# Optimization experiments

Measured on AMD Instinct MI355X. Metric: run time of the kernel, lower is better.

## Reference

```python
import jax, jax.numpy as jnp
import numpy as np

TAU = 2.0
V_TH = 1.0
V_RST = 0.0
BN_EPS = 1e-5

# --- ATan surrogate-gradient Heaviside spike (spikingjelly default, alpha=2) ---
@jax.custom_vjp
def atan_spike(x):
    return (x >= 0.0).astype(x.dtype)

def _atan_fwd(x):
    return atan_spike(x), x

def _atan_bwd(x, g):
    alpha = 2.0
    return (g * (alpha / 2.0) / (1.0 + (jnp.pi / 2.0 * alpha * x) ** 2),)

atan_spike.defvjp(_atan_fwd, _atan_bwd)

# --- multi-step LIF (decay_input=False, hard reset, detach_reset=True) ---
def lif(x_seq):
    def step(v, xt):
        v = v - (v - V_RST) / TAU + xt            # charge
        s = atan_spike(v - V_TH)                  # fire
        sd = jax.lax.stop_gradient(s)             # detach_reset
        v = (1.0 - sd) * v + sd * V_RST           # hard reset
        return v, s
    v0 = jnp.full(x_seq.shape[1:], V_RST, x_seq.dtype)
    _, spikes = jax.lax.scan(step, v0, x_seq)
    return spikes

def setup_inputs() -> dict:
    key = jax.random.key(0)
    k1, k2 = jax.random.split(key)
    T, B, N = 64, 256, 512
    x = jax.random.normal(k1, (T, B, N), dtype=jnp.float32)
    # xavier-uniform-like init for Linear weight [out, in]
    bound = float(np.sqrt(6.0 / (N + N)))
    W = jax.random.uniform(k2, (N, N), minval=-bound, maxval=bound, dtype=jnp.float32)
    gamma = jnp.ones((N,), jnp.float32)
    beta = jnp.zeros((N,), jnp.float32)
    return {"x": x, "W": W, "gamma": gamma, "beta": beta}

def reference(x, W, gamma, beta):
    # x: [T, B, N]
    T, B, N = x.shape
    # spatial / temporal spiking gates (reduction='mean')
    spatial = lif(x.mean(axis=-1, keepdims=True))   # [T, B, 1]
    temporal = lif(x.mean(axis=0, keepdims=True))   # [1, B, N] (scan over length-1 T)
    s = (x * spatial) * (x * temporal)
    x = x + s
    x = lif(x)
    # Linear (no bias): y = x @ W.T
    x = jnp.einsum('tbn,mn->tbm', x, W)
    # BatchNorm1d over channels N, stats over flattened T*B (training mode)
    xf = x.reshape(T * B, N)
    mu = xf.mean(axis=0)
    var = xf.var(axis=0)
    xf = (xf - mu) * jax.lax.rsqrt(var + BN_EPS) * gamma + beta
    x = xf.reshape(T, B, N)
    x = lif(x)
    return x
```

## Files before the change

### kernel.cpp

```cpp
#include <hip/hip_runtime.h>
#include <hip/hip_bf16.h>
#include <math.h>

#define TT 64
#define BB 256
#define NN 512

typedef __attribute__((ext_vector_type(8)))  short s16x8;
typedef __attribute__((ext_vector_type(16))) float f32x16;

__device__ __forceinline__ void gload16(const void* g, void* l) {
  __builtin_amdgcn_global_load_lds(
      (const __attribute__((address_space(1))) unsigned int*)g,
      (__attribute__((address_space(3))) unsigned int*)l, 16, 0, 0);
}


__global__ __launch_bounds__(256) void wprep_kernel(
    const float* __restrict__ W, unsigned short* __restrict__ WT) {
  int i = blockIdx.x * 256 + threadIdx.x;
  int m = i >> 9, k = i & 511;
  float v = W[i];
  unsigned u0 = __float_as_uint(v);
  unsigned h0 = (u0 + 0x7FFFu + ((u0 >> 16) & 1u)) >> 16;
  float f0 = __uint_as_float(h0 << 16);
  float r1 = v - f0;
  unsigned u1 = __float_as_uint(r1);
  unsigned h1 = (u1 + 0x7FFFu + ((u1 >> 16) & 1u)) >> 16;
  float f1 = __uint_as_float(h1 << 16);
  float r2 = r1 - f1;
  unsigned u2 = __float_as_uint(r2);
  unsigned h2 = (u2 + 0x7FFFu + ((u2 >> 16) & 1u)) >> 16;
  int cg = m >> 5, kc = k >> 4;
  size_t base = ((size_t)cg * 32 + kc) * 512
              + ((m & 31) + 32 * ((k >> 3) & 1)) * 8 + (k & 7);
  WT[base         ] = (unsigned short)h0;
  WT[base + 262144] = (unsigned short)h1;
  WT[base + 524288] = (unsigned short)h2;
}

__global__ __launch_bounds__(512) void frontend_kernel(
    const float* __restrict__ x, unsigned short* __restrict__ spkT) {
  extern __shared__ float xs[];
  __shared__ float rms[TT];
  __shared__ float sp[TT];
  int b = blockIdx.x, tid = threadIdx.x;
  int l = tid & 63, w = tid >> 6;
  #pragma unroll
  for (int p = 0; p < 16; ++p) {
    int f = p * 512 + tid;
    int t = f >> 7, c4 = f & 127;
    gload16(x + (size_t)t * (BB * NN) + (size_t)b * NN + c4 * 4,
            (char*)xs + p * 8192 + w * 1024);
  }
  __syncthreads();
  #pragma unroll
  for (int j = 0; j < 8; ++j) {
    int t = w * 8 + j;
    float s = 0.f;
    #pragma unroll
    for (int q = 0; q < 8; ++q) s += xs[t * 512 + q * 64 + l];
    #pragma unroll
    for (int off = 32; off; off >>= 1) s += __shfl_xor(s, off);
    if (l == 0) rms[t] = s;
  }
  float cs = 0.f;
  for (int t = 0; t < TT; ++t) cs += xs[t * 512 + tid];
  __syncthreads();
  if (w == 0) {
    float myrm = rms[l];
    float v = 0.f;
    unsigned long long mask = 0ull;
    #pragma unroll
    for (int t = 0; t < TT; ++t) {
      float m = __shfl(myrm, t) * (1.0f / 512.0f);
      v = v * 0.5f + m;
      if (v >= 1.0f) { mask |= (1ull << t); v = 0.f; }
    }
    sp[l] = (float)((mask >> l) & 1ull);
  }
  __syncthreads();
  float te = (cs * (1.0f / 64.0f) >= 1.0f) ? 1.0f : 0.0f;
  float v = 0.f;
  unsigned short* sb = spkT + (size_t)(b >> 5) * 16384 + (tid >> 4) * 512
                     + (b & 31) * 8 + ((tid >> 3) & 1) * 256 + (tid & 7);
  for (int t = 0; t < TT; ++t) {
    float xv = xs[t * 512 + tid];
    float a = xv + (xv * sp[t]) * (xv * te);
    v = v * 0.5f + a;
    unsigned short s = (v >= 1.0f) ? 0x3F80 : 0;
    sb[(size_t)t * 131072] = s;
    if (s) v = 0.f;
  }
}

__global__ __launch_bounds__(256) void gemm_kernel(
    const unsigned short* __restrict__ AT, const unsigned short* __restrict__ WT,
    float* __restrict__ C, float* __restrict__ pS, float* __restrict__ pQ) {
  __shared__ unsigned char sm[2][32768];
  int tid = threadIdx.x;
  int l = tid & 63, w = tid >> 6;
  int wr = w >> 1, wc = w & 1;
  int bx = blockIdx.x, by = blockIdx.y;
  int row0 = bx * 128, col0 = by * 128;
  int lr = l & 31, lh = l >> 5;

  f32x16 acc[2][2];
  #pragma unroll
  for (int f = 0; f < 2; ++f)
    #pragma unroll
    for (int g = 0; g < 2; ++g)
      #pragma unroll
      for (int j = 0; j < 16; ++j) acc[f][g][j] = 0.f;

  auto STAGE = [&](unsigned char* lbase, int kt) {
    #pragma unroll
    for (int j = 0; j < 2; ++j) {
      int c = j * 4 + w;
      int rg = bx * 4 + (c >> 1), kc = kt * 2 + (c & 1);
      gload16((const char*)AT + ((size_t)rg * 32 + kc) * 1024 + l * 16,
              lbase + c * 1024);
    }
    #pragma unroll
    for (int j = 0; j < 6; ++j) {
      int c = j * 4 + w;
      int comp = c >> 3, cg = (c >> 1) & 3, kc = kt * 2 + (c & 1);
      gload16((const char*)WT + (((size_t)comp * 16 + by * 4 + cg) * 32 + kc) * 1024 + l * 16,
              lbase + 8192 + c * 1024);
    }
  };

  STAGE(sm[0], 0);
  #pragma unroll
  for (int kt = 0; kt < 16; ++kt) {
    asm volatile("s_waitcnt lgkmcnt(0)" ::: "memory");
    asm volatile("s_waitcnt vmcnt(0)" ::: "memory");
    asm volatile("s_barrier" ::: "memory");
    if (kt < 15) STAGE(sm[(kt + 1) & 1], kt + 1);
    const unsigned char* bp = sm[kt & 1];
    #pragma unroll
    for (int kc2 = 0; kc2 < 2; ++kc2) {
      s16x8 a[2], bf[2][3];
      #pragma unroll
      for (int f = 0; f < 2; ++f)
        a[f] = *(const s16x8*)(bp + ((wr * 2 + f) * 2 + kc2) * 1024 + l * 16);
      #pragma unroll
      for (int g = 0; g < 2; ++g)
        #pragma unroll
        for (int c = 0; c < 3; ++c)
          bf[g][c] = *(const s16x8*)(bp + 8192 + ((c * 4 + wc * 2 + g) * 2 + kc2) * 1024 + l * 16);
      __builtin_amdgcn_s_setprio(1);
      #pragma unroll
      for (int c = 0; c < 3; ++c)
        #pragma unroll
        for (int f = 0; f < 2; ++f)
          #pragma unroll
          for (int g = 0; g < 2; ++g)
            acc[f][g] = __builtin_amdgcn_mfma_f32_32x32x16_bf16(a[f], bf[g][c], acc[f][g], 0, 0, 0);
      __builtin_amdgcn_s_setprio(0);
    }
  }

  #pragma unroll
  for (int g = 0; g < 2; ++g) {
    int col = col0 + wc * 64 + g * 32 + lr;
    float sy = 0.f, sq = 0.f;
    #pragma unroll
    for (int f = 0; f < 2; ++f)
      #pragma unroll
      for (int j = 0; j < 16; ++j) {
        float y = acc[f][g][j];
        int row = row0 + wr * 64 + f * 32 + (j & 3) + 8 * (j >> 2) + 4 * lh;
        C[(size_t)row * NN + col] = y;
        sy += y; sq += y * y;
      }
    sy += __shfl_xor(sy, 32);
    sq += __shfl_xor(sq, 32);
    if (lh == 0) {
      pS[(size_t)col * 256 + bx * 2 + wr] = sy;
      pQ[(size_t)col * 256 + bx * 2 + wr] = sq;
    }
  }
}

__global__ __launch_bounds__(512) void bnstatsB_kernel(
    const float* __restrict__ pS, const float* __restrict__ pQ,
    float* __restrict__ mu, float* __restrict__ inv) {
  int tid = threadIdx.x;
  int ch = blockIdx.x * 64 + (tid >> 3), p = tid & 7;
  const float* ps = pS + (size_t)ch * 256 + p * 32;
  const float* pq = pQ + (size_t)ch * 256 + p * 32;
  float s = 0.f, q = 0.f;
  #pragma unroll
  for (int i = 0; i < 32; ++i) { s += ps[i]; q += pq[i]; }
  #pragma unroll
  for (int off = 1; off < 8; off <<= 1) { s += __shfl_xor(s, off); q += __shfl_xor(q, off); }
  if (p == 0) {
    float mean = s * (1.0f / 16384.0f);
    float var  = q * (1.0f / 16384.0f) - mean * mean;
    mu[ch] = mean;
    inv[ch] = 1.0f / sqrtf(var + 1e-5f);
  }
}

__global__ __launch_bounds__(256) void final_kernel(
    float* __restrict__ y, const float* __restrict__ mu, const float* __restrict__ inv,
    const float* __restrict__ gamma, const float* __restrict__ beta) {
  int g = blockIdx.x * 256 + threadIdx.x;
  int b = g >> 9, m = g & 511;
  float MU = mu[m], IV = inv[m], G = gamma[m], BE = beta[m];
  float* p = y + (size_t)b * NN + m;
  const size_t st = (size_t)BB * NN;
  float buf[16], nxt[16];
  #pragma unroll
  for (int j = 0; j < 16; ++j) buf[j] = p[(size_t)j * st];
  float v = 0.f;
  #pragma unroll
  for (int t0 = 0; t0 < 64; t0 += 16) {
    if (t0 + 16 < 64) {
      #pragma unroll
      for (int j = 0; j < 16; ++j) nxt[j] = p[(size_t)(t0 + 16 + j) * st];
    }
    #pragma unroll
    for (int j = 0; j < 16; ++j) {
      float xb = (buf[j] - MU) * IV * G + BE;
      v = v * 0.5f + xb;
      float s = (v >= 1.0f) ? 1.0f : 0.0f;
      p[(size_t)(t0 + j) * st] = s;
      if (s != 0.f) v = 0.f;
    }
    #pragma unroll
    for (int j = 0; j < 16; ++j) buf[j] = nxt[j];
  }
}

extern "C" void kernel_launch(void* const* d_in, const int* in_sizes, int n_in,
                              void* d_out, int out_size, void* d_ws, size_t ws_size,
                              hipStream_t stream) {
  const float* x     = (const float*)d_in[0];
  const float* W     = (const float*)d_in[1];
  const float* gamma = (const float*)d_in[2];
  const float* beta  = (const float*)d_in[3];
  float* out = (float*)d_out;

  char* ws = (char*)d_ws;
  unsigned short* WT   = (unsigned short*)ws;
  unsigned short* spkT = (unsigned short*)(ws + 1572864);
  float* pS    = (float*)(ws + 18350080);
  float* pQ    = (float*)(ws + 18874368);
  float* bn_mu = (float*)(ws + 19398656);
  float* bn_inv= (float*)(ws + 19400704);

  wprep_kernel<<<dim3(1024), dim3(256), 0, stream>>>(W, WT);
  frontend_kernel<<<dim3(BB), dim3(512), 131072, stream>>>(x, spkT);
  gemm_kernel<<<dim3(128, 4), dim3(256), 0, stream>>>(spkT, WT, out, pS, pQ);
  bnstatsB_kernel<<<dim3(8), dim3(512), 0, stream>>>(pS, pQ, bn_mu, bn_inv);
  final_kernel<<<dim3(512), dim3(256), 0, stream>>>(out, bn_mu, bn_inv, gamma, beta);
}
```

Baseline: 145.7 us.

## Fuse all stages into one cooperative persistent kernel with grid syncs

```diff
diff --git a/kernel.cpp b/kernel.cpp
--- a/kernel.cpp
+++ b/kernel.cpp
@@ -1,6 +1,9 @@
 #include <hip/hip_runtime.h>
+#include <hip/hip_cooperative_groups.h>
 #include <hip/hip_bf16.h>
 #include <math.h>
+
+namespace cg = cooperative_groups;
 
 #define TT 64
 #define BB 256
@@ -15,222 +18,229 @@
       (__attribute__((address_space(3))) unsigned int*)l, 16, 0, 0);
 }
 
-
-__global__ __launch_bounds__(256) void wprep_kernel(
-    const float* __restrict__ W, unsigned short* __restrict__ WT) {
-  int i = blockIdx.x * 256 + threadIdx.x;
-  int m = i >> 9, k = i & 511;
-  float v = W[i];
-  unsigned u0 = __float_as_uint(v);
-  unsigned h0 = (u0 + 0x7FFFu + ((u0 >> 16) & 1u)) >> 16;
-  float f0 = __uint_as_float(h0 << 16);
-  float r1 = v - f0;
-  unsigned u1 = __float_as_uint(r1);
-  unsigned h1 = (u1 + 0x7FFFu + ((u1 >> 16) & 1u)) >> 16;
-  float f1 = __uint_as_float(h1 << 16);
-  float r2 = r1 - f1;
-  unsigned u2 = __float_as_uint(r2);
-  unsigned h2 = (u2 + 0x7FFFu + ((u2 >> 16) & 1u)) >> 16;
-  int cg = m >> 5, kc = k >> 4;
-  size_t base = ((size_t)cg * 32 + kc) * 512
-              + ((m & 31) + 32 * ((k >> 3) & 1)) * 8 + (k & 7);
-  WT[base         ] = (unsigned short)h0;
-  WT[base + 262144] = (unsigned short)h1;
-  WT[base + 524288] = (unsigned short)h2;
-}
-
-__global__ __launch_bounds__(512) void frontend_kernel(
-    const float* __restrict__ x, unsigned short* __restrict__ spkT) {
-  extern __shared__ float xs[];
+__device__ __forceinline__ unsigned bf16_rne(float v) {
+  unsigned u = __float_as_uint(v);
+  return (u + 0x7FFFu + ((u >> 16) & 1u)) >> 16;
+}
+
+__global__ __launch_bounds__(512) void mega_kernel(
+    const float* __restrict__ x, const float* __restrict__ W,
+    const float* __restrict__ gamma, const float* __restrict__ beta,
+    float* __restrict__ out, unsigned short* __restrict__ WT,
+    unsigned short* __restrict__ spkT, float* __restrict__ pS,
+    float* __restrict__ pQ, float* __restrict__ mu, float* __restrict__ inv) {
+  extern __shared__ char smem[];
   __shared__ float rms[TT];
   __shared__ float sp[TT];
-  int b = blockIdx.x, tid = threadIdx.x;
-  int l = tid & 63, w = tid >> 6;
-  #pragma unroll
-  for (int p = 0; p < 16; ++p) {
-    int f = p * 512 + tid;
-    int t = f >> 7, c4 = f & 127;
-    gload16(x + (size_t)t * (BB * NN) + (size_t)b * NN + c4 * 4,
-            (char*)xs + p * 8192 + w * 1024);
-  }
-  __syncthreads();
-  #pragma unroll
-  for (int j = 0; j < 8; ++j) {
-    int t = w * 8 + j;
-    float s = 0.f;
-    #pragma unroll
-    for (int q = 0; q < 8; ++q) s += xs[t * 512 + q * 64 + l];
-    #pragma unroll
-    for (int off = 32; off; off >>= 1) s += __shfl_xor(s, off);
-    if (l == 0) rms[t] = s;
-  }
-  float cs = 0.f;
-  for (int t = 0; t < TT; ++t) cs += xs[t * 512 + tid];
-  __syncthreads();
-  if (w == 0) {
-    float myrm = rms[l];
-    float v = 0.f;
-    unsigned long long mask = 0ull;
-    #pragma unroll
-    for (int t = 0; t < TT; ++t) {
-      float m = __shfl(myrm, t) * (1.0f / 512.0f);
-      v = v * 0.5f + m;
-      if (v >= 1.0f) { mask |= (1ull << t); v = 0.f; }
-    }
-    sp[l] = (float)((mask >> l) & 1ull);
-  }
-  __syncthreads();
-  float te = (cs * (1.0f / 64.0f) >= 1.0f) ? 1.0f : 0.0f;
-  float v = 0.f;
-  unsigned short* sb = spkT + (size_t)(b >> 5) * 16384 + (tid >> 4) * 512
-                     + (b & 31) * 8 + ((tid >> 3) & 1) * 256 + (tid & 7);
-  for (int t = 0; t < TT; ++t) {
-    float xv = xs[t * 512 + tid];
-    float a = xv + (xv * sp[t]) * (xv * te);
-    v = v * 0.5f + a;
-    unsigned short s = (v >= 1.0f) ? 0x3F80 : 0;
-    sb[(size_t)t * 131072] = s;
-    if (s) v = 0.f;
-  }
-}
-
-__global__ __launch_bounds__(256) void gemm_kernel(
-    const unsigned short* __restrict__ AT, const unsigned short* __restrict__ WT,
-    float* __restrict__ C, float* __restrict__ pS, float* __restrict__ pQ) {
-  __shared__ unsigned char sm[2][32768];
+  cg::grid_group grid = cg::this_grid();
   int tid = threadIdx.x;
   int l = tid & 63, w = tid >> 6;
-  int wr = w >> 1, wc = w & 1;
-  int bx = blockIdx.x, by = blockIdx.y;
-  int row0 = bx * 128, col0 = by * 128;
-  int lr = l & 31, lh = l >> 5;
-
-  f32x16 acc[2][2];
+  int blk = blockIdx.x;
+
   #pragma unroll
-  for (int f = 0; f < 2; ++f)
-    #pragma unroll
-    for (int g = 0; g < 2; ++g)
-      #pragma unroll
-      for (int j = 0; j < 16; ++j) acc[f][g][j] = 0.f;
-
-  auto STAGE = [&](unsigned char* lbase, int kt) {
-    #pragma unroll
-    for (int j = 0; j < 2; ++j) {
-      int c = j * 4 + w;
-      int rg = bx * 4 + (c >> 1), kc = kt * 2 + (c & 1);
-      gload16((const char*)AT + ((size_t)rg * 32 + kc) * 1024 + l * 16,
-              lbase + c * 1024);
-    }
-    #pragma unroll
-    for (int j = 0; j < 6; ++j) {
-      int c = j * 4 + w;
-      int comp = c >> 3, cg = (c >> 1) & 3, kc = kt * 2 + (c & 1);
-      gload16((const char*)WT + (((size_t)comp * 16 + by * 4 + cg) * 32 + kc) * 1024 + l * 16,
-              lbase + 8192 + c * 1024);
-    }
-  };
-
-  STAGE(sm[0], 0);
-  #pragma unroll
-  for (int kt = 0; kt < 16; ++kt) {
-    asm volatile("s_waitcnt lgkmcnt(0)" ::: "memory");
-    asm volatile("s_waitcnt vmcnt(0)" ::: "memory");
-    asm volatile("s_barrier" ::: "memory");
-    if (kt < 15) STAGE(sm[(kt + 1) & 1], kt + 1);
-    const unsigned char* bp = sm[kt & 1];
-    #pragma unroll
-    for (int kc2 = 0; kc2 < 2; ++kc2) {
-      s16x8 a[2], bf[2][3];
+  for (int r = 0; r < 2; ++r) {
+    int i = blk * 512 + tid + r * 131072;
+    int m = i >> 9, k = i & 511;
+    float v = W[i];
+    unsigned h0 = bf16_rne(v);
+    float f0 = __uint_as_float(h0 << 16);
+    float r1 = v - f0;
+    unsigned h1 = bf16_rne(r1);
+    float f1 = __uint_as_float(h1 << 16);
+    float r2 = r1 - f1;
+    unsigned h2 = bf16_rne(r2);
+    int cgp = m >> 5, kc = k >> 4;
+    size_t base = ((size_t)cgp * 32 + kc) * 512
+                + ((m & 31) + 32 * ((k >> 3) & 1)) * 8 + (k & 7);
+    WT[base         ] = (unsigned short)h0;
+    WT[base + 262144] = (unsigned short)h1;
+    WT[base + 524288] = (unsigned short)h2;
+  }
+
+  {
+    float* xs = (float*)smem;
+    int b = blk;
+    #pragma unroll
+    for (int p = 0; p < 16; ++p) {
+      int f = p * 512 + tid;
+      int t = f >> 7, c4 = f & 127;
+      gload16(x + (size_t)t * (BB * NN) + (size_t)b * NN + c4 * 4,
+              (char*)xs + p * 8192 + w * 1024);
+    }
+    __syncthreads();
+    #pragma unroll
+    for (int j = 0; j < 8; ++j) {
+      int t = w * 8 + j;
+      float s = 0.f;
+      #pragma unroll
+      for (int q = 0; q < 8; ++q) s += xs[t * 512 + q * 64 + l];
+      #pragma unroll
+      for (int off = 32; off; off >>= 1) s += __shfl_xor(s, off);
+      if (l == 0) rms[t] = s;
+    }
+    float cs = 0.f;
+    for (int t = 0; t < TT; ++t) cs += xs[t * 512 + tid];
+    __syncthreads();
+    if (w == 0) {
+      float myrm = rms[l];
+      float v = 0.f;
+      unsigned long long mask = 0ull;
+      #pragma unroll
+      for (int t = 0; t < TT; ++t) {
+        float m = __shfl(myrm, t) * (1.0f / 512.0f);
+        v = v * 0.5f + m;
+        if (v >= 1.0f) { mask |= (1ull << t); v = 0.f; }
+      }
+      sp[l] = (float)((mask >> l) & 1ull);
+    }
+    __syncthreads();
+    float te = (cs * (1.0f / 64.0f) >= 1.0f) ? 1.0f : 0.0f;
+    float v = 0.f;
+    unsigned short* sb = spkT + (size_t)(b >> 5) * 16384 + (tid >> 4) * 512
+                       + (b & 31) * 8 + ((tid >> 3) & 1) * 256 + (tid & 7);
+    for (int t = 0; t < TT; ++t) {
+      float xv = xs[t * 512 + tid];
+      float a = xv + (xv * sp[t]) * (xv * te);
+      v = v * 0.5f + a;
+      unsigned short s = (v >= 1.0f) ? 0x3F80 : 0;
+      sb[(size_t)t * 131072] = s;
+      if (s) v = 0.f;
+    }
+  }
+  __threadfence();
+  grid.sync();
+
+  {
+    unsigned char* sm0 = (unsigned char*)smem;
+    int nt = blk & 1, bx = blk >> 1;
+    int wr = w >> 2, wc = w & 3;
+    int lr = l & 31, lh = l >> 5;
+
+    f32x16 acc[2][2];
+    #pragma unroll
+    for (int f = 0; f < 2; ++f)
+      #pragma unroll
+      for (int g = 0; g < 2; ++g)
+        #pragma unroll
+        for (int j = 0; j < 16; ++j) acc[f][g][j] = 0.f;
+
+    auto STAGE = [&](unsigned char* lbase, int kt) {
+      #pragma unroll
+      for (int j = 0; j < 7; ++j) {
+        int cc = j * 8 + w;
+        if (cc < 8) {
+          int rg = bx * 4 + (cc >> 1), kc = kt * 2 + (cc & 1);
+          gload16((const char*)spkT + ((size_t)rg * 32 + kc) * 1024 + l * 16,
+                  lbase + cc * 1024);
+        } else {
+          int bb = cc - 8;
+          int comp = bb >> 4, cgl = (bb >> 1) & 7, kc2 = bb & 1;
+          gload16((const char*)WT + (size_t)comp * 524288
+                    + (((size_t)(nt * 8 + cgl) * 32) + kt * 2 + kc2) * 1024 + l * 16,
+                  lbase + 8192 + bb * 1024);
+        }
+      }
+    };
+
+    STAGE(sm0, 0);
+    for (int kt = 0; kt < 16; ++kt) {
+      asm volatile("s_waitcnt lgkmcnt(0)" ::: "memory");
+      asm volatile("s_waitcnt vmcnt(0)" ::: "memory");
+      __builtin_amdgcn_s_barrier();
+      if (kt < 15) STAGE(sm0 + ((kt + 1) & 1) * 57344, kt + 1);
+      const unsigned char* bp = sm0 + (kt & 1) * 57344;
+      #pragma unroll
+      for (int kc2 = 0; kc2 < 2; ++kc2) {
+        s16x8 a[2], bf[2][3];
+        #pragma unroll
+        for (int f = 0; f < 2; ++f)
+          a[f] = *(const s16x8*)(bp + ((wr * 2 + f) * 2 + kc2) * 1024 + l * 16);
+        #pragma unroll
+        for (int g = 0; g < 2; ++g)
+          #pragma unroll
+          for (int c = 0; c < 3; ++c)
+            bf[g][c] = *(const s16x8*)(bp + 8192 + ((size_t)((c * 8 + wc * 2 + g) * 2 + kc2)) * 1024 + l * 16);
+        __builtin_amdgcn_s_setprio(1);
+        #pragma unroll
+        for (int c = 0; c < 3; ++c)
+          #pragma unroll
+          for (int f = 0; f < 2; ++f)
+            #pragma unroll
+            for (int g = 0; g < 2; ++g)
+              acc[f][g] = __builtin_amdgcn_mfma_f32_32x32x16_bf16(a[f], bf[g][c], acc[f][g], 0, 0, 0);
+        __builtin_amdgcn_s_setprio(0);
+      }
+    }
+
+    #pragma unroll
+    for (int g = 0; g < 2; ++g) {
+      int col = nt * 256 + wc * 64 + g * 32 + lr;
+      float sy = 0.f, sq = 0.f;
       #pragma unroll
       for (int f = 0; f < 2; ++f)
-        a[f] = *(const s16x8*)(bp + ((wr * 2 + f) * 2 + kc2) * 1024 + l * 16);
-      #pragma unroll
-      for (int g = 0; g < 2; ++g)
-        #pragma unroll
-        for (int c = 0; c < 3; ++c)
-          bf[g][c] = *(const s16x8*)(bp + 8192 + ((c * 4 + wc * 2 + g) * 2 + kc2) * 1024 + l * 16);
-      __builtin_amdgcn_s_setprio(1);
-      #pragma unroll
-      for (int c = 0; c < 3; ++c)
-        #pragma unroll
-        for (int f = 0; f < 2; ++f)
-          #pragma unroll
-          for (int g = 0; g < 2; ++g)
-            acc[f][g] = __builtin_amdgcn_mfma_f32_32x32x16_bf16(a[f], bf[g][c], acc[f][g], 0, 0, 0);
-      __builtin_amdgcn_s_setprio(0);
-    }
-  }
-
-  #pragma unroll
-  for (int g = 0; g < 2; ++g) {
-    int col = col0 + wc * 64 + g * 32 + lr;
-    float sy = 0.f, sq = 0.f;
-    #pragma unroll
-    for (int f = 0; f < 2; ++f)
+        #pragma unroll
+        for (int j = 0; j < 16; ++j) {
+          float y = acc[f][g][j];
+          int row = bx * 128 + wr * 64 + f * 32 + (j & 3) + 8 * (j >> 2) + 4 * lh;
+          out[(size_t)row * NN + col] = y;
+          sy += y; sq += y * y;
+        }
+      sy += __shfl_xor(sy, 32);
+      sq += __shfl_xor(sq, 32);
+      if (lh == 0) {
+        pS[(size_t)col * 256 + bx * 2 + wr] = sy;
+        pQ[(size_t)col * 256 + bx * 2 + wr] = sq;
+      }
+    }
+  }
+  __threadfence();
+  grid.sync();
+
+  if (tid < 128) {
+    int ch = blk * 2 + (tid >> 6), ll = tid & 63;
+    const float* ps = pS + (size_t)ch * 256;
+    const float* pq = pQ + (size_t)ch * 256;
+    float s = (ps[ll] + ps[ll + 64]) + (ps[ll + 128] + ps[ll + 192]);
+    float q = (pq[ll] + pq[ll + 64]) + (pq[ll + 128] + pq[ll + 192]);
+    #pragma unroll
+    for (int off = 32; off; off >>= 1) { s += __shfl_xor(s, off); q += __shfl_xor(q, off); }
+    if (ll == 0) {
+      float mean = s * (1.0f / 16384.0f);
+      float var  = q * (1.0f / 16384.0f) - mean * mean;
+      mu[ch] = mean;
+      inv[ch] = 1.0f / sqrtf(var + 1e-5f);
+    }
+  }
+  __threadfence();
+  grid.sync();
+
+  {
+    int g = blk * 512 + tid;
+    int b = g >> 9, m = g & 511;
+    float MU = mu[m], IV = inv[m], G = gamma[m], BE = beta[m];
+    float* p = out + (size_t)b * NN + m;
+    const size_t st = (size_t)BB * NN;
+    float buf[16], nxt[16];
+    #pragma unroll
+    for (int j = 0; j < 16; ++j) buf[j] = p[(size_t)j * st];
+    float v = 0.f;
+    #pragma unroll
+    for (int t0 = 0; t0 < 64; t0 += 16) {
+      if (t0 + 16 < 64) {
+        #pragma unroll
+        for (int j = 0; j < 16; ++j) nxt[j] = p[(size_t)(t0 + 16 + j) * st];
+      }
       #pragma unroll
       for (int j = 0; j < 16; ++j) {
-        float y = acc[f][g][j];
-        int row = row0 + wr * 64 + f * 32 + (j & 3) + 8 * (j >> 2) + 4 * lh;
-        C[(size_t)row * NN + col] = y;
-        sy += y; sq += y * y;
-      }
-    sy += __shfl_xor(sy, 32);
-    sq += __shfl_xor(sq, 32);
-    if (lh == 0) {
-      pS[(size_t)col * 256 + bx * 2 + wr] = sy;
-      pQ[(size_t)col * 256 + bx * 2 + wr] = sq;
-    }
-  }
-}
-
-__global__ __launch_bounds__(512) void bnstatsB_kernel(
-    const float* __restrict__ pS, const float* __restrict__ pQ,
-    float* __restrict__ mu, float* __restrict__ inv) {
-  int tid = threadIdx.x;
-  int ch = blockIdx.x * 64 + (tid >> 3), p = tid & 7;
-  const float* ps = pS + (size_t)ch * 256 + p * 32;
-  const float* pq = pQ + (size_t)ch * 256 + p * 32;
-  float s = 0.f, q = 0.f;
-  #pragma unroll
-  for (int i = 0; i < 32; ++i) { s += ps[i]; q += pq[i]; }
-  #pragma unroll
-  for (int off = 1; off < 8; off <<= 1) { s += __shfl_xor(s, off); q += __shfl_xor(q, off); }
-  if (p == 0) {
-    float mean = s * (1.0f / 16384.0f);
-    float var  = q * (1.0f / 16384.0f) - mean * mean;
-    mu[ch] = mean;
-    inv[ch] = 1.0f / sqrtf(var + 1e-5f);
-  }
-}
-
-__global__ __launch_bounds__(256) void final_kernel(
-    float* __restrict__ y, const float* __restrict__ mu, const float* __restrict__ inv,
-    const float* __restrict__ gamma, const float* __restrict__ beta) {
-  int g = blockIdx.x * 256 + threadIdx.x;
-  int b = g >> 9, m = g & 511;
-  float MU = mu[m], IV = inv[m], G = gamma[m], BE = beta[m];
-  float* p = y + (size_t)b * NN + m;
-  const size_t st = (size_t)BB * NN;
-  float buf[16], nxt[16];
-  #pragma unroll
-  for (int j = 0; j < 16; ++j) buf[j] = p[(size_t)j * st];
-  float v = 0.f;
-  #pragma unroll
-  for (int t0 = 0; t0 < 64; t0 += 16) {
-    if (t0 + 16 < 64) {
-      #pragma unroll
-      for (int j = 0; j < 16; ++j) nxt[j] = p[(size_t)(t0 + 16 + j) * st];
-    }
-    #pragma unroll
-    for (int j = 0; j < 16; ++j) {
-      float xb = (buf[j] - MU) * IV * G + BE;
-      v = v * 0.5f + xb;
-      float s = (v >= 1.0f) ? 1.0f : 0.0f;
-      p[(size_t)(t0 + j) * st] = s;
-      if (s != 0.f) v = 0.f;
-    }
-    #pragma unroll
-    for (int j = 0; j < 16; ++j) buf[j] = nxt[j];
+        float xb = (buf[j] - MU) * IV * G + BE;
+        v = v * 0.5f + xb;
+        float s = (v >= 1.0f) ? 1.0f : 0.0f;
+        p[(size_t)(t0 + j) * st] = s;
+        if (s != 0.f) v = 0.f;
+      }
+      #pragma unroll
+      for (int j = 0; j < 16; ++j) buf[j] = nxt[j];
+    }
   }
 }
 
@@ -251,9 +261,9 @@
   float* bn_mu = (float*)(ws + 19398656);
   float* bn_inv= (float*)(ws + 19400704);
 
-  wprep_kernel<<<dim3(1024), dim3(256), 0, stream>>>(W, WT);
-  frontend_kernel<<<dim3(BB), dim3(512), 131072, stream>>>(x, spkT);
-  gemm_kernel<<<dim3(128, 4), dim3(256), 0, stream>>>(spkT, WT, out, pS, pQ);
-  bnstatsB_kernel<<<dim3(8), dim3(512), 0, stream>>>(pS, pQ, bn_mu, bn_inv);
-  final_kernel<<<dim3(512), dim3(256), 0, stream>>>(out, bn_mu, bn_inv, gamma, beta);
-}
+  void* args[] = {(void*)&x, (void*)&W, (void*)&gamma, (void*)&beta,
+                  (void*)&out, (void*)&WT, (void*)&spkT, (void*)&pS,
+                  (void*)&pQ, (void*)&bn_mu, (void*)&bn_inv};
+  hipLaunchCooperativeKernel((void*)mega_kernel, dim3(256), dim3(512),
+                             args, 131072, stream);
+}
```

New measurement: 420.7 us. 189% more time.
